# Performance work log

Measured on AMD Instinct MI355X. Metric: run time of the kernel, lower is better.

The kernel has to match this reference:

```python
import jax, jax.numpy as jnp
import numpy as np

N_NODES = 100000
N_EDGES = 6400000
GAIN_BASE = 10.0


def setup_inputs() -> dict:
    key = jax.random.key(0)
    ks = jax.random.split(key, 9)
    rates = jax.random.normal(ks[0], (N_NODES,), dtype=jnp.float32)
    weights = jax.random.normal(ks[1], (N_EDGES,), dtype=jnp.float32) * 0.1
    gain = jax.random.uniform(ks[2], (N_NODES,), dtype=jnp.float32) * 0.5  # gain_base**gain stays moderate
    time_constant = jax.random.uniform(ks[3], (N_NODES,), dtype=jnp.float32) + 0.5  # in [0.5, 1.5]
    baseline = jax.random.normal(ks[4], (N_NODES,), dtype=jnp.float32) * 0.1
    ext_input = jax.random.normal(ks[5], (N_NODES,), dtype=jnp.float32)
    src = jax.random.randint(ks[6], (N_EDGES,), 0, N_NODES, dtype=jnp.int32)
    dst = jax.random.randint(ks[7], (N_EDGES,), 0, N_NODES, dtype=jnp.int32)
    is_input = jax.random.randint(ks[8], (N_NODES,), 0, 2) > 0
    return {
        "rates": rates, "weights": weights, "gain": gain,
        "time_constant": time_constant, "baseline": baseline,
        "ext_input": ext_input, "src": src, "dst": dst, "is_input": is_input,
    }


def reference(rates, weights, gain, time_constant, baseline, ext_input, src, dst, is_input):
    # synaptic_input[v] = sum over incoming edges (u->v) of rates[u] * weight(u,v)
    messages = rates[src] * weights                      # [E] gather + multiply
    syn = jax.ops.segment_sum(messages, dst, num_segments=N_NODES)  # [N]
    # input nodes get external input only; others get synaptic input
    total = jnp.where(is_input, ext_input, syn) + baseline
    act = jnp.tanh(total)
    # dr/dt = (1/tau) * (-r + gain_base**gain * activation(input))
    return (-rates + jnp.power(GAIN_BASE, gain) * act) / time_constant
```

## Files before the change

### kernel.cpp

```cpp
#include <hip/hip_runtime.h>
#include <math.h>

#define N_NODES 100000
#define N_EDGES 6400000
#define K_BINS  5
#define BIN_SZ  20000
#define BLOCK   1024
#define LOG2_10 3.321928094887362f

__global__ __launch_bounds__(BLOCK) void edge_bin_kernel(
        const float* __restrict__ rates,
        const float* __restrict__ weights,
        const int* __restrict__ src,
        const int* __restrict__ dst,
        float* __restrict__ part,
        int n_chunks, int edges_per_chunk) {
    __shared__ float bin[BIN_SZ];
    const int b = blockIdx.x % K_BINS;
    const int c = blockIdx.x / K_BINS;
    const int base_node = b * BIN_SZ;

    for (int i = threadIdx.x; i < BIN_SZ; i += BLOCK) bin[i] = 0.0f;
    __syncthreads();

    const long e0 = (long)c * edges_per_chunk;
    const int nvec = edges_per_chunk >> 2;
    const int4*   s4 = (const int4*)(src + e0);
    const int4*   d4 = (const int4*)(dst + e0);
    const float4* w4 = (const float4*)(weights + e0);

    for (int i = threadIdx.x; i < nvec; i += BLOCK) {
        int4   d = d4[i];
        int4   s = s4[i];
        float4 w = w4[i];
        unsigned dx = (unsigned)(d.x - base_node);
        unsigned dy = (unsigned)(d.y - base_node);
        unsigned dz = (unsigned)(d.z - base_node);
        unsigned dw = (unsigned)(d.w - base_node);
        if (dx < BIN_SZ) atomicAdd(&bin[dx], rates[s.x] * w.x);
        if (dy < BIN_SZ) atomicAdd(&bin[dy], rates[s.y] * w.y);
        if (dz < BIN_SZ) atomicAdd(&bin[dz], rates[s.z] * w.z);
        if (dw < BIN_SZ) atomicAdd(&bin[dw], rates[s.w] * w.w);
    }
    __syncthreads();

    float4* outp = (float4*)(part + (size_t)c * N_NODES + base_node);
    for (int i = threadIdx.x; i < (BIN_SZ >> 2); i += BLOCK) {
        outp[i] = make_float4(bin[4*i], bin[4*i+1], bin[4*i+2], bin[4*i+3]);
    }
}

__global__ void node_kernel(const float* __restrict__ rates,
                            const float* __restrict__ gain,
                            const float* __restrict__ time_constant,
                            const float* __restrict__ baseline,
                            const float* __restrict__ ext_input,
                            const int*   __restrict__ is_input,
                            const float* __restrict__ part,
                            float* __restrict__ out,
                            int n_chunks) {
    int v = blockIdx.x * blockDim.x + threadIdx.x;
    if (v >= N_NODES) return;
    float s0 = 0.0f, s1 = 0.0f, s2 = 0.0f, s3 = 0.0f;
    int k = 0;
    for (; k + 3 < n_chunks; k += 4) {
        s0 += part[(size_t)(k + 0) * N_NODES + v];
        s1 += part[(size_t)(k + 1) * N_NODES + v];
        s2 += part[(size_t)(k + 2) * N_NODES + v];
        s3 += part[(size_t)(k + 3) * N_NODES + v];
    }
    for (; k < n_chunks; ++k) s0 += part[(size_t)k * N_NODES + v];
    float s = (s0 + s1) + (s2 + s3);
    float total = (is_input[v] != 0 ? ext_input[v] : s) + baseline[v];
    float act = tanhf(total);
    float g = exp2f(gain[v] * LOG2_10);
    out[v] = (-rates[v] + g * act) / time_constant[v];
}

extern "C" void kernel_launch(void* const* d_in, const int* in_sizes, int n_in,
                              void* d_out, int out_size, void* d_ws, size_t ws_size,
                              hipStream_t stream) {
    const float* rates         = (const float*)d_in[0];
    const float* weights       = (const float*)d_in[1];
    const float* gain          = (const float*)d_in[2];
    const float* time_constant = (const float*)d_in[3];
    const float* baseline      = (const float*)d_in[4];
    const float* ext_input     = (const float*)d_in[5];
    const int*   src           = (const int*)d_in[6];
    const int*   dst           = (const int*)d_in[7];
    const int*   is_input      = (const int*)d_in[8];
    float* out  = (float*)d_out;
    float* part = (float*)d_ws;

    static const int cand[] = {100, 50, 25, 20, 10, 5, 4, 2, 1};
    int n_chunks = 1;
    for (int i = 0; i < (int)(sizeof(cand)/sizeof(cand[0])); ++i) {
        if ((size_t)cand[i] * N_NODES * sizeof(float) <= ws_size) { n_chunks = cand[i]; break; }
    }
    int edges_per_chunk = N_EDGES / n_chunks;

    int grid_e = K_BINS * n_chunks;
    edge_bin_kernel<<<grid_e, BLOCK, 0, stream>>>(rates, weights, src, dst,
                                                  part, n_chunks, edges_per_chunk);

    int block = 256;
    int grid_n = (N_NODES + block - 1) / block;
    node_kernel<<<grid_n, block, 0, stream>>>(rates, gain, time_constant, baseline,
                                              ext_input, is_input, part, out, n_chunks);
}
```

Measured before the change: 187.7 us.

## Bucket edges by destination bin once, then scatter packed fp16 records per bin

Replaces the kernel where every bin block re-read all edges of its chunk with two passes. The first pass reads each edge once, computes the message, and writes it into one of five per-bin buckets as a packed record: a 16-bit local node offset plus the message in fp16. Slots are reserved with wave ballots and shared plus global counters. The second pass has each bin/chunk block read only its bucket's records and accumulate them into LDS. This removes the five-fold redundant reads of src, dst and weights. In exchange it adds an extra write/read of bucket data and ballot overhead, loses precision by storing messages in fp16, and silently drops edges if a bin exceeds the fixed capacity sized for a roughly uniform dst distribution.

```diff
diff --git a/kernel.cpp b/kernel.cpp
--- a/kernel.cpp
+++ b/kernel.cpp
@@ -1,53 +1,135 @@
 #include <hip/hip_runtime.h>
+#include <hip/hip_fp16.h>
 #include <math.h>
 
 #define N_NODES 100000
 #define N_EDGES 6400000
+#define NVEC    (N_EDGES / 4)
 #define K_BINS  5
 #define BIN_SZ  20000
-#define BLOCK   1024
+#define P1_BLOCK 1024
+#define P1_VEC   2048
 #define LOG2_10 3.321928094887362f
 
-__global__ __launch_bounds__(BLOCK) void edge_bin_kernel(
+__global__ __launch_bounds__(P1_BLOCK) void bucket_kernel(
         const float* __restrict__ rates,
         const float* __restrict__ weights,
         const int* __restrict__ src,
         const int* __restrict__ dst,
+        unsigned* __restrict__ buckets,
+        unsigned* __restrict__ cursor,
+        unsigned cap) {
+    __shared__ unsigned cnt[K_BINS], gbase[K_BINS], wcur[K_BINS];
+    const int tid  = threadIdx.x;
+    const int lane = tid & 63;
+    const unsigned long long lt = (1ULL << lane) - 1ULL;
+
+    if (tid < K_BINS) { cnt[tid] = 0; wcur[tid] = 0; }
+    __syncthreads();
+
+    int bins[8]; unsigned recs[8];
+    #pragma unroll
+    for (int s = 0; s < 2; ++s) {
+        long i = (long)blockIdx.x * P1_VEC + s * P1_BLOCK + tid;
+        if (i < NVEC) {
+            int4   sv = ((const int4*)src)[i];
+            int4   dv = ((const int4*)dst)[i];
+            float4 wv = ((const float4*)weights)[i];
+            int   dd[4] = {dv.x, dv.y, dv.z, dv.w};
+            int   ss[4] = {sv.x, sv.y, sv.z, sv.w};
+            float ww[4] = {wv.x, wv.y, wv.z, wv.w};
+            #pragma unroll
+            for (int j = 0; j < 4; ++j) {
+                int b = dd[j] / BIN_SZ;
+                unsigned h = (unsigned)__half_as_ushort(__float2half(rates[ss[j]] * ww[j]));
+                bins[s * 4 + j] = b;
+                recs[s * 4 + j] = ((unsigned)(dd[j] - b * BIN_SZ) << 16) | h;
+            }
+        } else {
+            #pragma unroll
+            for (int j = 0; j < 4; ++j) bins[s * 4 + j] = -1;
+        }
+    }
+
+    #pragma unroll
+    for (int j = 0; j < 8; ++j) {
+        #pragma unroll
+        for (int b = 0; b < K_BINS; ++b) {
+            unsigned long long m = __ballot(bins[j] == b);
+            if (bins[j] == b) {
+                if (lane == __ffsll((unsigned long long)m) - 1)
+                    atomicAdd(&cnt[b], (unsigned)__popcll(m));
+            }
+        }
+    }
+    __syncthreads();
+    if (tid < K_BINS) gbase[tid] = atomicAdd(&cursor[tid], cnt[tid]);
+    __syncthreads();
+
+    #pragma unroll
+    for (int j = 0; j < 8; ++j) {
+        #pragma unroll
+        for (int b = 0; b < K_BINS; ++b) {
+            unsigned long long m = __ballot(bins[j] == b);
+            if (bins[j] == b) {
+                int leader = __ffsll((unsigned long long)m) - 1;
+                unsigned wb = 0;
+                if (lane == leader) wb = atomicAdd(&wcur[b], (unsigned)__popcll(m));
+                wb = __shfl(wb, leader);
+                unsigned p = gbase[b] + wb + (unsigned)__popcll(m & lt);
+                if (p < cap) buckets[(size_t)b * cap + p] = recs[j];
+            }
+        }
+    }
+}
+
+__global__ __launch_bounds__(1024) void scatter_kernel(
+        const unsigned* __restrict__ buckets,
+        const unsigned* __restrict__ cursor,
+        unsigned cap,
         float* __restrict__ part,
-        int n_chunks, int edges_per_chunk) {
+        int n_chunks) {
     __shared__ float bin[BIN_SZ];
     const int b = blockIdx.x % K_BINS;
     const int c = blockIdx.x / K_BINS;
-    const int base_node = b * BIN_SZ;
-
-    for (int i = threadIdx.x; i < BIN_SZ; i += BLOCK) bin[i] = 0.0f;
-    __syncthreads();
-
-    const long e0 = (long)c * edges_per_chunk;
-    const int nvec = edges_per_chunk >> 2;
-    const int4*   s4 = (const int4*)(src + e0);
-    const int4*   d4 = (const int4*)(dst + e0);
-    const float4* w4 = (const float4*)(weights + e0);
-
-    for (int i = threadIdx.x; i < nvec; i += BLOCK) {
-        int4   d = d4[i];
-        int4   s = s4[i];
-        float4 w = w4[i];
-        unsigned dx = (unsigned)(d.x - base_node);
-        unsigned dy = (unsigned)(d.y - base_node);
-        unsigned dz = (unsigned)(d.z - base_node);
-        unsigned dw = (unsigned)(d.w - base_node);
-        if (dx < BIN_SZ) atomicAdd(&bin[dx], rates[s.x] * w.x);
-        if (dy < BIN_SZ) atomicAdd(&bin[dy], rates[s.y] * w.y);
-        if (dz < BIN_SZ) atomicAdd(&bin[dz], rates[s.z] * w.z);
-        if (dw < BIN_SZ) atomicAdd(&bin[dw], rates[s.w] * w.w);
-    }
-    __syncthreads();
-
-    float4* outp = (float4*)(part + (size_t)c * N_NODES + base_node);
-    for (int i = threadIdx.x; i < (BIN_SZ >> 2); i += BLOCK) {
+    unsigned len = cursor[b]; if (len > cap) len = cap;
+
+    for (int i = threadIdx.x; i < BIN_SZ; i += 1024) bin[i] = 0.0f;
+    __syncthreads();
+
+    const unsigned* rec = buckets + (size_t)b * cap;
+    unsigned nv = (len + 3) >> 2;
+    size_t v0 = (size_t)nv * c / n_chunks;
+    size_t v1 = (size_t)nv * (c + 1) / n_chunks;
+    for (size_t i = v0 + threadIdx.x; i < v1; i += 1024) {
+        uint4 r = ((const uint4*)rec)[i];
+        size_t e = i * 4;
+        if (e + 0 < len) atomicAdd(&bin[r.x >> 16], __half2float(__ushort_as_half((unsigned short)(r.x & 0xffffu))));
+        if (e + 1 < len) atomicAdd(&bin[r.y >> 16], __half2float(__ushort_as_half((unsigned short)(r.y & 0xffffu))));
+        if (e + 2 < len) atomicAdd(&bin[r.z >> 16], __half2float(__ushort_as_half((unsigned short)(r.z & 0xffffu))));
+        if (e + 3 < len) atomicAdd(&bin[r.w >> 16], __half2float(__ushort_as_half((unsigned short)(r.w & 0xffffu))));
+    }
+    __syncthreads();
+
+    float4* outp = (float4*)(part + (size_t)c * N_NODES + b * BIN_SZ);
+    for (int i = threadIdx.x; i < (BIN_SZ >> 2); i += 1024)
         outp[i] = make_float4(bin[4*i], bin[4*i+1], bin[4*i+2], bin[4*i+3]);
-    }
+}
+
+__global__ void fallback_edge_kernel(const float* __restrict__ rates,
+                                     const float* __restrict__ weights,
+                                     const int* __restrict__ src,
+                                     const int* __restrict__ dst,
+                                     float* __restrict__ syn) {
+    int i = blockIdx.x * blockDim.x + threadIdx.x;
+    if (i >= NVEC) return;
+    int4   s = ((const int4*)src)[i];
+    int4   d = ((const int4*)dst)[i];
+    float4 w = ((const float4*)weights)[i];
+    atomicAdd(&syn[d.x], rates[s.x] * w.x);
+    atomicAdd(&syn[d.y], rates[s.y] * w.y);
+    atomicAdd(&syn[d.z], rates[s.z] * w.z);
+    atomicAdd(&syn[d.w], rates[s.w] * w.w);
 }
 
 __global__ void node_kernel(const float* __restrict__ rates,
@@ -89,22 +171,45 @@
     const int*   src           = (const int*)d_in[6];
     const int*   dst           = (const int*)d_in[7];
     const int*   is_input      = (const int*)d_in[8];
-    float* out  = (float*)d_out;
-    float* part = (float*)d_ws;
-
-    static const int cand[] = {100, 50, 25, 20, 10, 5, 4, 2, 1};
-    int n_chunks = 1;
-    for (int i = 0; i < (int)(sizeof(cand)/sizeof(cand[0])); ++i) {
-        if ((size_t)cand[i] * N_NODES * sizeof(float) <= ws_size) { n_chunks = cand[i]; break; }
-    }
-    int edges_per_chunk = N_EDGES / n_chunks;
-
-    int grid_e = K_BINS * n_chunks;
-    edge_bin_kernel<<<grid_e, BLOCK, 0, stream>>>(rates, weights, src, dst,
-                                                  part, n_chunks, edges_per_chunk);
-
+    float* out = (float*)d_out;
+
+    unsigned* cursor = (unsigned*)d_ws;
+
+    unsigned cap = 1400000;
+    size_t avail = (ws_size > 256) ? ws_size - 256 : 0;
+    while (cap > 1320000 &&
+           (size_t)K_BINS * cap * 4 + (size_t)N_NODES * 4 > avail)
+        cap -= 8000;
+
+    bool have_room = ((size_t)K_BINS * cap * 4 + (size_t)N_NODES * 4 <= avail);
     int block = 256;
     int grid_n = (N_NODES + block - 1) / block;
+
+    if (!have_room) {
+        float* syn = (float*)((char*)d_ws + 256);
+        hipMemsetAsync(syn, 0, (size_t)N_NODES * sizeof(float), stream);
+        fallback_edge_kernel<<<(NVEC + 255) / 256, 256, 0, stream>>>(rates, weights, src, dst, syn);
+        node_kernel<<<grid_n, block, 0, stream>>>(rates, gain, time_constant, baseline,
+                                                  ext_input, is_input, syn, out, 1);
+        return;
+    }
+
+    unsigned* buckets = (unsigned*)((char*)d_ws + 256);
+    float* part = (float*)((char*)d_ws + 256 + (size_t)K_BINS * cap * 4);
+    size_t part_avail = avail - (size_t)K_BINS * cap * 4;
+    int n_chunks = (int)(part_avail / ((size_t)N_NODES * 4));
+    if (n_chunks > 104) n_chunks = 104;
+    if (n_chunks < 1) n_chunks = 1;
+
+    hipMemsetAsync(cursor, 0, K_BINS * sizeof(unsigned), stream);
+
+    int grid1 = (NVEC + P1_VEC - 1) / P1_VEC;
+    bucket_kernel<<<grid1, P1_BLOCK, 0, stream>>>(rates, weights, src, dst,
+                                                  buckets, cursor, cap);
+
+    scatter_kernel<<<K_BINS * n_chunks, 1024, 0, stream>>>(buckets, cursor, cap,
+                                                           part, n_chunks);
+
     node_kernel<<<grid_n, block, 0, stream>>>(rates, gain, time_constant, baseline,
                                               ext_input, is_input, part, out, n_chunks);
 }
```

Measured after the change: 266.5 us. +42.0%, slower.
